# Kernel optimization log

Measured on AMD Instinct MI355X. Metric: run time of the kernel, lower is better.

The kernel has to match this reference:

```python
import jax, jax.numpy as jnp
import numpy as np

NUM_HEADS = 16

def setup_inputs() -> dict:
    key = jax.random.key(0)
    ks = jax.random.split(key, 9)
    B, S, H = 2, 2048, 1024
    sc = 0.02
    return {
        "x":  jax.random.normal(ks[0], (B, S, H), jnp.float32),
        "Wq": jax.random.normal(ks[1], (H, H), jnp.float32) * sc,
        "bq": jnp.zeros((H,), jnp.float32),
        "Wk": jax.random.normal(ks[2], (H, H), jnp.float32) * sc,
        "bk": jnp.zeros((H,), jnp.float32),
        "Wv": jax.random.normal(ks[3], (H, H), jnp.float32) * sc,
        "bv": jnp.zeros((H,), jnp.float32),
        "Wo": jax.random.normal(ks[4], (H, H), jnp.float32) * sc,
        "bo": jnp.zeros((H,), jnp.float32),
    }

def _split_heads(t, nh):
    B, S, H = t.shape
    return t.reshape(B, S, nh, H // nh).transpose(0, 2, 1, 3)  # [B, nh, S, hd]

def reference(x, Wq, bq, Wk, bk, Wv, bv, Wo, bo):
    # mask_type == 'gaussian', dropout = 0 (eval), return_weights = False
    B, S, H = x.shape
    nh = NUM_HEADS
    q = _split_heads(x @ Wq + bq, nh)  # [B, nh, S, hd]
    k = _split_heads(x @ Wk + bk, nh)
    v = _split_heads(x @ Wv + bv, nh)
    dif = q - k  # elementwise, as in the original
    # exp(-dif @ dif^T / 2)
    score = jnp.exp(-0.5 * jnp.einsum('bhqd,bhkd->bhqk', dif, dif))
    # gaussian mask: 1 strictly above the diagonal, 0 on/below (faithful to source)
    mask = jnp.triu(jnp.ones((S, S), x.dtype), k=1)
    prob = score * mask  # [B, nh, S, S]
    ctx = jnp.einsum('bhqk,bhkd->bhqd', prob, v)  # [B, nh, S, hd]
    ctx = ctx.transpose(0, 2, 1, 3).reshape(B, S, H)
    return ctx @ Wo + bo
```

## Files before the change

### kernel.cpp

```cpp
#include <hip/hip_runtime.h>
#include <math.h>

constexpr int SEQ  = 2048;
constexpr int HID  = 1024;
constexpr int MTOT = 4096;
constexpr int BH   = 32;

typedef _Float16 f16;
typedef _Float16 f16x8 __attribute__((ext_vector_type(8)));
typedef float    f32x4 __attribute__((ext_vector_type(4)));

__device__ __forceinline__ void gld16(const f16* g, f16* l) {
    __builtin_amdgcn_global_load_lds(
        (__attribute__((address_space(1))) void*)g,
        (__attribute__((address_space(3))) void*)l, 16, 0, 0);
}

__global__ __launch_bounds__(256) void prep(const float* __restrict__ x,
                                            const float* __restrict__ Wq,
                                            const float* __restrict__ Wk,
                                            const float* __restrict__ Wv,
                                            const float* __restrict__ Wo,
                                            f16* __restrict__ xh,
                                            f16* __restrict__ WqkT,
                                            f16* __restrict__ WvT,
                                            f16* __restrict__ WoT) {
    __shared__ f16 T[64][72];
    const int z = blockIdx.z;
    const int t = threadIdx.x;

    if (z == 3) {
        const int chunk = blockIdx.y * 16 + blockIdx.x;
        const float* src = x + (size_t)chunk * 16384;
        f16* dst = xh + (size_t)chunk * 16384;
#pragma unroll
        for (int it = 0; it < 16; it++) {
            const int i = it * 1024 + t * 4;
            float4 v = *(const float4*)(src + i);
            f16 o[4] = {(f16)v.x, (f16)v.y, (f16)v.z, (f16)v.w};
            *(ushort4*)(dst + i) = *(ushort4*)o;
        }
        return;
    }

    const float* W  = (z == 0) ? Wq : (z == 1) ? Wv : Wo;
    f16* WT = (z == 0) ? WqkT : (z == 1) ? WvT : WoT;
    const int k0 = blockIdx.x * 64, n0 = blockIdx.y * 64;
    const int r  = t >> 4;
    const int c4 = (t & 15) * 4;
#pragma unroll
    for (int rr = 0; rr < 64; rr += 16) {
        float4 w = *(const float4*)(W + (size_t)(k0 + rr + r) * HID + n0 + c4);
        if (z == 0) {
            float4 w2 = *(const float4*)(Wk + (size_t)(k0 + rr + r) * HID + n0 + c4);
            w.x -= w2.x; w.y -= w2.y; w.z -= w2.z; w.w -= w2.w;
        }
        T[c4 + 0][rr + r] = (f16)w.x;
        T[c4 + 1][rr + r] = (f16)w.y;
        T[c4 + 2][rr + r] = (f16)w.z;
        T[c4 + 3][rr + r] = (f16)w.w;
    }
    __syncthreads();
#pragma unroll
    for (int pp = 0; pp < 2; pp++) {
        const int nr = pp * 32 + (t >> 3);
        const int kc = (t & 7) * 8;
        *(uint4*)(WT + (size_t)(n0 + nr) * HID + k0 + kc) = *(uint4*)(&T[nr][kc]);
    }
}

__global__ __launch_bounds__(256, 4) void proj_gemm(const f16* __restrict__ A,
                                                    const f16* __restrict__ WqkT,
                                                    const f16* __restrict__ WvT,
                                                    const float* __restrict__ bq,
                                                    const float* __restrict__ bk,
                                                    const float* __restrict__ bv,
                                                    f16* __restrict__ dif,
                                                    f16* __restrict__ vT) {
    __shared__ f16 As[128 * 72];
    __shared__ f16 Bs[64 * 64];
    const int t = threadIdx.x;
    const int m0  = blockIdx.x * 128;
    const int n0g = blockIdx.y * 64;
    const bool isv = (n0g >= HID);
    const f16* BT = isv ? WvT : WqkT;
    const int n0 = n0g & (HID - 1);
    const int w = t >> 6, l = t & 63, quad = l >> 4, ln = l & 15;
    const int wm = w * 32;
    const int xk = ln & 7;

    const int srow8 = l >> 3;
    const int soct  = (l & 7) ^ srow8;
    const f16* pa = A  + (size_t)(m0 + w * 32 + srow8) * HID + soct * 8;
    const f16* pb = BT + (size_t)(n0 + w * 16 + srow8) * HID + soct * 8;

    f32x4 acc[2][4] = {};

    for (int k0 = 0; k0 < HID; k0 += 64) {
        __syncthreads();
#pragma unroll
        for (int c = 0; c < 4; c++)
            gld16(pa + (size_t)c * 8 * HID + k0, As + (w * 4 + c) * 512);
#pragma unroll
        for (int c = 0; c < 2; c++)
            gld16(pb + (size_t)c * 8 * HID + k0, Bs + (w * 2 + c) * 512);
        __syncthreads();

#pragma unroll
        for (int kh = 0; kh < 2; kh++) {
            f16x8 af[2], bf[4];
#pragma unroll
            for (int mt = 0; mt < 2; mt++) {
                const int row = wm + mt * 16 + ln;
                const int oct = (kh * 4 + quad) ^ xk;
                af[mt] = *(const f16x8*)(As + row * 64 + oct * 8);
            }
#pragma unroll
            for (int nt = 0; nt < 4; nt++) {
                const int row = nt * 16 + ln;
                const int oct = (kh * 4 + quad) ^ xk;
                bf[nt] = *(const f16x8*)(Bs + row * 64 + oct * 8);
            }
#pragma unroll
            for (int mt = 0; mt < 2; mt++)
#pragma unroll
                for (int nt = 0; nt < 4; nt++)
                    acc[mt][nt] = __builtin_amdgcn_mfma_f32_16x16x32_f16(
                        af[mt], bf[nt], acc[mt][nt], 0, 0, 0);
        }
    }

    __syncthreads();
    const int b_  = m0 >> 11;
    const int s0g = m0 & 2047;
    const int h_  = n0 >> 6;

    if (!isv) {
        float bb[4];
#pragma unroll
        for (int nt = 0; nt < 4; nt++) {
            const int nl = n0 + nt * 16 + ln;
            bb[nt] = bq[nl] - bk[nl];
        }
#pragma unroll
        for (int mt = 0; mt < 2; mt++)
#pragma unroll
            for (int nt = 0; nt < 4; nt++)
#pragma unroll
                for (int r = 0; r < 4; r++) {
                    const int sl = wm + mt * 16 + quad * 4 + r;
                    As[sl * 72 + nt * 16 + ln] = (f16)(acc[mt][nt][r] + bb[nt]);
                }
        __syncthreads();
        f16* base = dif + ((size_t)(b_ * 16 + h_) * SEQ + s0g) * 64;
        const int sl = t >> 1, eo = (t & 1) * 32;
#pragma unroll
        for (int i = 0; i < 4; i++)
            *(uint4*)(base + (size_t)sl * 64 + eo + i * 8) =
                *(uint4*)(&As[sl * 72 + eo + i * 8]);
    } else {
        float bb[4];
#pragma unroll
        for (int nt = 0; nt < 4; nt++)
            bb[nt] = bv[n0 + nt * 16 + ln];
#pragma unroll
        for (int mt = 0; mt < 2; mt++)
#pragma unroll
            for (int nt = 0; nt < 4; nt++)
#pragma unroll
                for (int r = 0; r < 4; r++) {
                    const int sl = wm + mt * 16 + quad * 4 + r;
                    As[(nt * 16 + ln) * 136 + sl] = (f16)(acc[mt][nt][r] + bb[nt]);
                }
        __syncthreads();
        const int eb = t >> 2, so = (t & 3) * 32;
        f16* base = vT + ((size_t)(b_ * 16 + h_) * 64 + eb) * SEQ + s0g + so;
#pragma unroll
        for (int i = 0; i < 4; i++)
            *(uint4*)(base + i * 8) = *(uint4*)(&As[eb * 136 + so + i * 8]);
    }
}

__global__ __launch_bounds__(256) void out_gemm(const f16* __restrict__ C0,
                                                const f16* __restrict__ C1,
                                                const f16* __restrict__ WoT,
                                                const float* __restrict__ bo,
                                                float* __restrict__ out) {
    __shared__ f16 As[2][128 * 72];
    __shared__ f16 Bs[2][64 * 72];
    const int t = threadIdx.x;
    const int m0 = blockIdx.x * 128, n0 = blockIdx.y * 64;
    const int w = t >> 6, l = t & 63, quad = l >> 4, ln = l & 15;
    const int wm = (w >> 1) * 64, wn = (w & 1) * 32;
    const int arow = t >> 1, ahalf = (t & 1) * 32;
    const int brow = t >> 2, boff = (t & 3) * 16;

    const f16* pa0 = C0  + (size_t)(m0 + arow) * HID + ahalf;
    const f16* pa1 = C1  + (size_t)(m0 + arow) * HID + ahalf;
    const f16* pb  = WoT + (size_t)(n0 + brow) * HID + boff;

    f16x8 a0 = *(const f16x8*)(pa0)      + *(const f16x8*)(pa1);
    f16x8 a1 = *(const f16x8*)(pa0 + 8)  + *(const f16x8*)(pa1 + 8);
    f16x8 a2 = *(const f16x8*)(pa0 + 16) + *(const f16x8*)(pa1 + 16);
    f16x8 a3 = *(const f16x8*)(pa0 + 24) + *(const f16x8*)(pa1 + 24);
    uint4 b0 = *(const uint4*)(pb), b1 = *(const uint4*)(pb + 8);

    f32x4 acc[4][2] = {};
    int buf = 0;

    for (int k0 = 0; k0 < HID; k0 += 64) {
        f16* da = As[buf] + arow * 72 + ahalf;
        *(f16x8*)(da)      = a0; *(f16x8*)(da + 8)  = a1;
        *(f16x8*)(da + 16) = a2; *(f16x8*)(da + 24) = a3;
        f16* db = Bs[buf] + brow * 72 + boff;
        *(uint4*)(db) = b0; *(uint4*)(db + 8) = b1;
        __syncthreads();
        if (k0 + 64 < HID) {
            const int kn = k0 + 64;
            a0 = *(const f16x8*)(pa0 + kn)      + *(const f16x8*)(pa1 + kn);
            a1 = *(const f16x8*)(pa0 + kn + 8)  + *(const f16x8*)(pa1 + kn + 8);
            a2 = *(const f16x8*)(pa0 + kn + 16) + *(const f16x8*)(pa1 + kn + 16);
            a3 = *(const f16x8*)(pa0 + kn + 24) + *(const f16x8*)(pa1 + kn + 24);
            b0 = *(const uint4*)(pb + kn); b1 = *(const uint4*)(pb + kn + 8);
        }
#pragma unroll
        for (int kh = 0; kh < 2; kh++) {
            f16x8 af[4], bf[2];
#pragma unroll
            for (int mt = 0; mt < 4; mt++)
                af[mt] = *(const f16x8*)(As[buf] + (wm + mt * 16 + ln) * 72 + kh * 32 + quad * 8);
#pragma unroll
            for (int nt = 0; nt < 2; nt++)
                bf[nt] = *(const f16x8*)(Bs[buf] + (wn + nt * 16 + ln) * 72 + kh * 32 + quad * 8);
#pragma unroll
            for (int mt = 0; mt < 4; mt++)
#pragma unroll
                for (int nt = 0; nt < 2; nt++)
                    acc[mt][nt] = __builtin_amdgcn_mfma_f32_16x16x32_f16(
                        af[mt], bf[nt], acc[mt][nt], 0, 0, 0);
        }
        buf ^= 1;
    }

#pragma unroll
    for (int mt = 0; mt < 4; mt++)
#pragma unroll
        for (int nt = 0; nt < 2; nt++) {
            const int n = n0 + wn + nt * 16 + ln;
            const float bb = bo[n];
            const int m_base = m0 + wm + mt * 16 + quad * 4;
#pragma unroll
            for (int r = 0; r < 4; r++)
                out[(size_t)(m_base + r) * HID + n] =
                    acc[mt][nt][r] * 65536.0f + bb;
        }
}

__global__ __launch_bounds__(256, 4) void attn_f16(const f16* __restrict__ dif,
                                                   const f16* __restrict__ vT,
                                                   f16* __restrict__ ctx0,
                                                   f16* __restrict__ ctx1) {
    __shared__ f16 Qs[64 * 72];
    __shared__ f16 Ks[64 * 72];
    __shared__ f16 Vs[64 * 72];
    __shared__ f16 Ps[64 * 72];

    const int pq = blockIdx.x, bh = blockIdx.y, ks = blockIdx.z;
    f16* Cout = ks ? ctx1 : ctx0;
    const f16* D  = dif + (size_t)bh * SEQ * 64;
    const f16* VT = vT  + (size_t)bh * 64 * SEQ;
    const int b = bh >> 4, h = bh & 15;
    const int t = threadIdx.x, w = t >> 6, l = t & 63, quad = l >> 4, ln = l & 15;
    const int qh = w >> 1, jh = w & 1;
    const int ve = t >> 2, vc = (t & 3) * 16;

    for (int half = 0; half < 2; half++) {
        const int qt = half ? (31 - pq) : pq;
        const int i0 = qt * 64;
        __syncthreads();

#pragma unroll
        for (int rr = 0; rr < 2; rr++) {
            const int o = rr * 2048 + t * 8;
            uint4 v = *(const uint4*)(D + i0 * 64 + o);
            *(uint4*)(Qs + (o >> 6) * 72 + (o & 63)) = v;
        }
        __syncthreads();
        f16x8 aq[2][2];
#pragma unroll
        for (int mt = 0; mt < 2; mt++)
#pragma unroll
            for (int kh = 0; kh < 2; kh++)
                aq[mt][kh] = *(const f16x8*)(Qs + (qh * 32 + mt * 16 + ln) * 72
                                             + kh * 32 + quad * 8);

        f32x4 acc[2][4] = {};
        const int kt0 = qt + ks;

        uint4 kr0, kr1, vr0, vr1;
        if (kt0 < 32) {
            const int j0 = kt0 * 64;
            kr0 = *(const uint4*)(D + j0 * 64 + t * 8);
            kr1 = *(const uint4*)(D + j0 * 64 + 2048 + t * 8);
            vr0 = *(const uint4*)(VT + (size_t)ve * SEQ + j0 + vc);
            vr1 = *(const uint4*)(VT + (size_t)ve * SEQ + j0 + vc + 8);
        }

        for (int kt = kt0; kt < 32; kt += 2) {
            const int j0 = kt * 64;
            __syncthreads();

            {
                const int o0 = t * 8, o1 = 2048 + t * 8;
                *(uint4*)(Ks + (o0 >> 6) * 72 + (o0 & 63)) = kr0;
                *(uint4*)(Ks + (o1 >> 6) * 72 + (o1 & 63)) = kr1;
                *(uint4*)(Vs + ve * 72 + vc)     = vr0;
                *(uint4*)(Vs + ve * 72 + vc + 8) = vr1;
            }
            __syncthreads();

            if (kt + 2 < 32) {
                const int j2 = (kt + 2) * 64;
                kr0 = *(const uint4*)(D + j2 * 64 + t * 8);
                kr1 = *(const uint4*)(D + j2 * 64 + 2048 + t * 8);
                vr0 = *(const uint4*)(VT + (size_t)ve * SEQ + j2 + vc);
                vr1 = *(const uint4*)(VT + (size_t)ve * SEQ + j2 + vc + 8);
            }

            f32x4 st[2][2] = {};
#pragma unroll
            for (int kh = 0; kh < 2; kh++)
#pragma unroll
                for (int nt = 0; nt < 2; nt++) {
                    f16x8 ak = *(const f16x8*)(Ks + (jh * 32 + nt * 16 + ln) * 72
                                               + kh * 32 + quad * 8);
#pragma unroll
                    for (int mt = 0; mt < 2; mt++)
                        st[nt][mt] = __builtin_amdgcn_mfma_f32_16x16x32_f16(
                            ak, aq[mt][kh], st[nt][mt], 0, 0, 0);
                }

            const bool full = (kt > qt);
#pragma unroll
            for (int nt = 0; nt < 2; nt++)
#pragma unroll
                for (int mt = 0; mt < 2; mt++) {
                    const int gi = i0 + qh * 32 + mt * 16 + ln;
                    f16 pv4[4];
#pragma unroll
                    for (int r = 0; r < 4; r++) {
                        const int gj = j0 + jh * 32 + nt * 16 + quad * 4 + r;
                        float p = (full || (gj > gi))
                                      ? fminf(__expf(fmaf(st[nt][mt][r], -0.5f,
                                                          -11.090354888959125f)),
                                              60000.0f)
                                      : 0.0f;
                        pv4[r] = (f16)p;
                    }
                    *(double*)(Ps + (qh * 32 + mt * 16 + ln) * 72
                               + jh * 32 + nt * 16 + quad * 4) = *(double*)pv4;
                }

            {
                f16x8 bv[4];
#pragma unroll
                for (int nt = 0; nt < 4; nt++)
                    bv[nt] = *(const f16x8*)(Vs + (nt * 16 + ln) * 72
                                             + jh * 32 + quad * 8);
#pragma unroll
                for (int mt = 0; mt < 2; mt++) {
                    f16x8 ap = *(const f16x8*)(Ps + (qh * 32 + mt * 16 + ln) * 72
                                               + jh * 32 + quad * 8);
#pragma unroll
                    for (int nt = 0; nt < 4; nt++)
                        acc[mt][nt] = __builtin_amdgcn_mfma_f32_16x16x32_f16(
                            ap, bv[nt], acc[mt][nt], 0, 0, 0);
                }
            }
        }

        __syncthreads();
        if (jh == 1) {
#pragma unroll
            for (int mt = 0; mt < 2; mt++)
#pragma unroll
                for (int nt = 0; nt < 4; nt++)
#pragma unroll
                    for (int r = 0; r < 4; r++)
                        Ps[(qh * 32 + mt * 16 + quad * 4 + r) * 72 + nt * 16 + ln] =
                            (f16)acc[mt][nt][r];
        }
        __syncthreads();
        if (jh == 0) {
#pragma unroll
            for (int mt = 0; mt < 2; mt++)
#pragma unroll
                for (int nt = 0; nt < 4; nt++)
#pragma unroll
                    for (int r = 0; r < 4; r++) {
                        const int iloc = qh * 32 + mt * 16 + quad * 4 + r;
                        float v = acc[mt][nt][r]
                                + (float)Ps[iloc * 72 + nt * 16 + ln];
                        Cout[(size_t)(b * SEQ + i0 + iloc) * HID + h * 64
                             + nt * 16 + ln] = (f16)v;
                    }
        }
    }
}

extern "C" void kernel_launch(void* const* d_in, const int* in_sizes, int n_in,
                              void* d_out, int out_size, void* d_ws, size_t ws_size,
                              hipStream_t stream) {
    const float* x  = (const float*)d_in[0];
    const float* Wq = (const float*)d_in[1];
    const float* bq = (const float*)d_in[2];
    const float* Wk = (const float*)d_in[3];
    const float* bk = (const float*)d_in[4];
    const float* Wv = (const float*)d_in[5];
    const float* bv = (const float*)d_in[6];
    const float* Wo = (const float*)d_in[7];
    const float* bo = (const float*)d_in[8];
    float* out = (float*)d_out;

    char* ws = (char*)d_ws;
    f16* xh   = (f16*)(ws);
    f16* WqkT = (f16*)(ws + (8 << 20));
    f16* WvT  = (f16*)(ws + (10 << 20));
    f16* WoT  = (f16*)(ws + (12 << 20));
    f16* dif  = (f16*)(ws + (14 << 20));
    f16* vT   = (f16*)(ws + (22 << 20));
    f16* ctx0 = (f16*)(ws + (30 << 20));
    f16* ctx1 = (f16*)(ws + (38 << 20));

    prep<<<dim3(16, 16, 4), 256, 0, stream>>>(x, Wq, Wk, Wv, Wo,
                                              xh, WqkT, WvT, WoT);
    proj_gemm<<<dim3(MTOT / 128, 32), 256, 0, stream>>>(xh, WqkT, WvT,
                                                        bq, bk, bv, dif, vT);
    attn_f16<<<dim3(16, BH, 2), 256, 0, stream>>>(dif, vT, ctx0, ctx1);
    out_gemm<<<dim3(MTOT / 128, 16), 256, 0, stream>>>(ctx0, ctx1, WoT, bo, out);
}
```

Baseline: 188.0 us.

## Keep attention probabilities in registers and remap grid for L2 locality

The attention kernel no longer writes the probability tile to shared memory and reads it back. Instead it feeds the register-resident score fragments straight into 16x16x16 MFMA as the A operand, which matches the accumulator layout, and drops the Ps buffer (the epilogue now reuses Qs). The launch also becomes a 1D grid with a custom block-to-(bh, query tile, k-split) mapping, intended to spread heads across XCDs. The trade-off is twice as many smaller MFMA instructions in exchange for less LDS traffic, fewer LDS round trips and a smaller shared-memory footprint.

```diff
diff --git a/kernel.cpp b/kernel.cpp
--- a/kernel.cpp
+++ b/kernel.cpp
@@ -7,6 +7,7 @@
 constexpr int BH   = 32;
 
 typedef _Float16 f16;
+typedef _Float16 f16x4 __attribute__((ext_vector_type(4)));
 typedef _Float16 f16x8 __attribute__((ext_vector_type(8)));
 typedef float    f32x4 __attribute__((ext_vector_type(4)));
 
@@ -263,9 +264,13 @@
     __shared__ f16 Qs[64 * 72];
     __shared__ f16 Ks[64 * 72];
     __shared__ f16 Vs[64 * 72];
-    __shared__ f16 Ps[64 * 72];
-
-    const int pq = blockIdx.x, bh = blockIdx.y, ks = blockIdx.z;
+
+    const int blk = blockIdx.x;
+    const int g   = blk >> 3;
+    const int bh  = (blk & 7) * 4 + (g & 3);
+    const int pq  = (g >> 2) & 15;
+    const int ks  = g >> 6;
+
     f16* Cout = ks ? ctx1 : ctx0;
     const f16* D  = dif + (size_t)bh * SEQ * 64;
     const f16* VT = vT  + (size_t)bh * 64 * SEQ;
@@ -341,12 +346,12 @@
                 }
 
             const bool full = (kt > qt);
+            f16x4 pf[2][2];
 #pragma unroll
             for (int nt = 0; nt < 2; nt++)
 #pragma unroll
                 for (int mt = 0; mt < 2; mt++) {
                     const int gi = i0 + qh * 32 + mt * 16 + ln;
-                    f16 pv4[4];
 #pragma unroll
                     for (int r = 0; r < 4; r++) {
                         const int gj = j0 + jh * 32 + nt * 16 + quad * 4 + r;
@@ -355,28 +360,21 @@
                                                           -11.090354888959125f)),
                                               60000.0f)
                                       : 0.0f;
-                        pv4[r] = (f16)p;
+                        pf[nt][mt][r] = (f16)p;
                     }
-                    *(double*)(Ps + (qh * 32 + mt * 16 + ln) * 72
-                               + jh * 32 + nt * 16 + quad * 4) = *(double*)pv4;
                 }
 
-            {
-                f16x8 bv[4];
-#pragma unroll
-                for (int nt = 0; nt < 4; nt++)
-                    bv[nt] = *(const f16x8*)(Vs + (nt * 16 + ln) * 72
-                                             + jh * 32 + quad * 8);
-#pragma unroll
-                for (int mt = 0; mt < 2; mt++) {
-                    f16x8 ap = *(const f16x8*)(Ps + (qh * 32 + mt * 16 + ln) * 72
-                                               + jh * 32 + quad * 8);
-#pragma unroll
-                    for (int nt = 0; nt < 4; nt++)
-                        acc[mt][nt] = __builtin_amdgcn_mfma_f32_16x16x32_f16(
-                            ap, bv[nt], acc[mt][nt], 0, 0, 0);
+#pragma unroll
+            for (int nt = 0; nt < 2; nt++)
+#pragma unroll
+                for (int nte = 0; nte < 4; nte++) {
+                    f16x4 bv = *(const f16x4*)(Vs + (nte * 16 + ln) * 72
+                                               + jh * 32 + nt * 16 + quad * 4);
+#pragma unroll
+                    for (int mt = 0; mt < 2; mt++)
+                        acc[mt][nte] = __builtin_amdgcn_mfma_f32_16x16x16f16(
+                            pf[nt][mt], bv, acc[mt][nte], 0, 0, 0);
                 }
-            }
         }
 
         __syncthreads();
@@ -384,25 +382,25 @@
 #pragma unroll
             for (int mt = 0; mt < 2; mt++)
 #pragma unroll
-                for (int nt = 0; nt < 4; nt++)
+                for (int nte = 0; nte < 4; nte++)
 #pragma unroll
                     for (int r = 0; r < 4; r++)
-                        Ps[(qh * 32 + mt * 16 + quad * 4 + r) * 72 + nt * 16 + ln] =
-                            (f16)acc[mt][nt][r];
+                        Qs[(qh * 32 + mt * 16 + quad * 4 + r) * 72 + nte * 16 + ln] =
+                            (f16)acc[mt][nte][r];
         }
         __syncthreads();
         if (jh == 0) {
 #pragma unroll
             for (int mt = 0; mt < 2; mt++)
 #pragma unroll
-                for (int nt = 0; nt < 4; nt++)
+                for (int nte = 0; nte < 4; nte++)
 #pragma unroll
                     for (int r = 0; r < 4; r++) {
                         const int iloc = qh * 32 + mt * 16 + quad * 4 + r;
-                        float v = acc[mt][nt][r]
-                                + (float)Ps[iloc * 72 + nt * 16 + ln];
+                        float v = acc[mt][nte][r]
+                                + (float)Qs[iloc * 72 + nte * 16 + ln];
                         Cout[(size_t)(b * SEQ + i0 + iloc) * HID + h * 64
-                             + nt * 16 + ln] = (f16)v;
+                             + nte * 16 + ln] = (f16)v;
                     }
         }
     }
@@ -436,6 +434,6 @@
                                               xh, WqkT, WvT, WoT);
     proj_gemm<<<dim3(MTOT / 128, 32), 256, 0, stream>>>(xh, WqkT, WvT,
                                                         bq, bk, bv, dif, vT);
-    attn_f16<<<dim3(16, BH, 2), 256, 0, stream>>>(dif, vT, ctx0, ctx1);
+    attn_f16<<<1024, 256, 0, stream>>>(dif, vT, ctx0, ctx1);
     out_gemm<<<dim3(MTOT / 128, 16), 256, 0, stream>>>(ctx0, ctx1, WoT, bo, out);
 }
```

Measured after the change: 185.8 us. Within noise of the previous version (-1.2%).
